# Performance work log

Hardware: AMD Instinct MI355X
Metric: run time of the kernel (lower is better)

## Reference

```python
import jax, jax.numpy as jnp
import numpy as np

N_NODES = 50000
N_EDGES = 800000
IN_CH = 128
HIDDEN = 32
HEADS = 4
OUT_CH = 128


def _lin_params(key, fan_in, fan_out):
    kw, kb = jax.random.split(key)
    scale = 1.0 / np.sqrt(fan_in)
    W = jax.random.uniform(kw, (fan_in, fan_out), minval=-scale, maxval=scale, dtype=jnp.float32)
    b = jax.random.uniform(kb, (fan_out,), minval=-scale, maxval=scale, dtype=jnp.float32)
    return W, b


def setup_inputs() -> dict:
    key = jax.random.key(0)
    ks = jax.random.split(key, 10)
    x = jax.random.normal(ks[0], (N_NODES, IN_CH), dtype=jnp.float32)
    edge_index = jax.random.randint(ks[1], (2, N_EDGES), 0, N_NODES, dtype=jnp.int64)
    d1 = HIDDEN * HEADS  # 128
    Wq1, bq1 = _lin_params(ks[2], IN_CH, d1)
    Wk1, bk1 = _lin_params(ks[3], IN_CH, d1)
    Wv1, bv1 = _lin_params(ks[4], IN_CH, d1)
    Ws1, bs1 = _lin_params(ks[5], IN_CH, d1)
    Wq2, bq2 = _lin_params(ks[6], d1, OUT_CH)
    Wk2, bk2 = _lin_params(ks[7], d1, OUT_CH)
    Wv2, bv2 = _lin_params(ks[8], d1, OUT_CH)
    Ws2, bs2 = _lin_params(ks[9], d1, OUT_CH)
    return dict(x=x, edge_index=edge_index,
                Wq1=Wq1, bq1=bq1, Wk1=Wk1, bk1=bk1, Wv1=Wv1, bv1=bv1, Ws1=Ws1, bs1=bs1,
                Wq2=Wq2, bq2=bq2, Wk2=Wk2, bk2=bk2, Wv2=Wv2, bv2=bv2, Ws2=Ws2, bs2=bs2)


def transformer_conv(x, src, dst, Wq, bq, Wk, bk, Wv, bv, Ws, bs, heads, n_nodes):
    """PyG TransformerConv (concat=True, beta=False, root_weight=True, dropout=0)."""
    H = heads
    d = Wq.shape[1] // H
    q = (x @ Wq + bq).reshape(n_nodes, H, d)  # [N,H,d]
    k = (x @ Wk + bk).reshape(n_nodes, H, d)
    v = (x @ Wv + bv).reshape(n_nodes, H, d)
    q_e = q[dst]          # [E,H,d] gather by destination (x_i)
    k_e = k[src]          # [E,H,d] gather by source (x_j)
    alpha = jnp.einsum('ehd,ehd->eh', q_e, k_e) / jnp.sqrt(jnp.float32(d))  # [E,H]
    # segment softmax over incoming edges of each destination node
    m = jax.ops.segment_max(alpha, dst, num_segments=n_nodes)  # [N,H]
    m = jnp.where(jnp.isfinite(m), m, 0.0)
    e = jnp.exp(alpha - m[dst])
    denom = jax.ops.segment_sum(e, dst, num_segments=n_nodes)  # [N,H]
    attn = e / (denom[dst] + 1e-16)                            # [E,H]
    msg = v[src] * attn[:, :, None]                            # [E,H,d]
    out = jax.ops.segment_sum(msg, dst, num_segments=n_nodes)  # [N,H,d]
    out = out.reshape(n_nodes, H * d)
    return out + (x @ Ws + bs)  # root/skip connection


def reference(x, edge_index, Wq1, bq1, Wk1, bk1, Wv1, bv1, Ws1, bs1,
              Wq2, bq2, Wk2, bk2, Wv2, bv2, Ws2, bs2):
    src = edge_index[0]
    dst = edge_index[1]
    n = x.shape[0]
    h = transformer_conv(x, src, dst, Wq1, bq1, Wk1, bk1, Wv1, bv1, Ws1, bs1, HEADS, n)
    h = jax.nn.relu(h)
    out = transformer_conv(h, src, dst, Wq2, bq2, Wk2, bk2, Wv2, bv2, Ws2, bs2, 1, n)
    return out
```

## Files before the change

kernel.cpp:

```cpp
#include <hip/hip_runtime.h>

#define N_NODES 50000
#define N_EDGES 800000

typedef __attribute__((ext_vector_type(8))) short bf16x8;
typedef __attribute__((ext_vector_type(4))) float f32x4;

__device__ inline unsigned short f2bf(float f) {
  unsigned int u = __float_as_uint(f);
  unsigned int r = u + 0x7FFFu + ((u >> 16) & 1u);
  return (unsigned short)(r >> 16);
}
__device__ inline float bf_lo(unsigned int u) { return __uint_as_float(u << 16); }
__device__ inline float bf_hi(unsigned int u) { return __uint_as_float(u & 0xffff0000u); }

__global__ void edges_prep(const int* __restrict__ ei,
                           int* __restrict__ src, int* __restrict__ dst,
                           int* __restrict__ cnt) {
  int e = blockIdx.x * 256 + threadIdx.x;
  int hi = ei[2 * e + 1];
  unsigned long long b = __ballot(hi == 0);
  bool is64 = (b == 0xFFFFFFFFFFFFFFFFull);
  int s, d;
  if (is64) { s = ei[2 * e]; d = ei[2 * (N_EDGES + e)]; }
  else      { s = ei[e];     d = ei[N_EDGES + e]; }
  src[e] = s; dst[e] = d;
  atomicAdd(&cnt[d], 1);
}

__device__ inline int block_excl_scan_256(int v, int& total) {
  __shared__ int lds[8];
  int lane = threadIdx.x & 63, wid = threadIdx.x >> 6;
  int orig = v;
#pragma unroll
  for (int off = 1; off < 64; off <<= 1) {
    int t = __shfl_up(v, off);
    if (lane >= off) v += t;
  }
  if (lane == 63) lds[wid] = v;
  __syncthreads();
  if (threadIdx.x == 0) {
    int s = 0;
    for (int w = 0; w < 4; ++w) { int t = lds[w]; lds[w] = s; s += t; }
    lds[4] = s;
  }
  __syncthreads();
  total = lds[4];
  return v + lds[wid] - orig;
}

__global__ __launch_bounds__(256) void scan1(const int* __restrict__ cnt,
                                             int* __restrict__ excl,
                                             int* __restrict__ partials) {
  int i = blockIdx.x * 256 + threadIdx.x;
  int v = (i < N_NODES) ? cnt[i] : 0;
  int total;
  int e = block_excl_scan_256(v, total);
  if (i < N_NODES) excl[i] = e;
  if (threadIdx.x == 0) partials[blockIdx.x] = total;
}

__global__ __launch_bounds__(256) void scan2(int* __restrict__ partials, int nb) {
  int i = threadIdx.x;
  int v = (i < nb) ? partials[i] : 0;
  int total;
  int e = block_excl_scan_256(v, total);
  if (i < nb) partials[i] = e;
}

__global__ __launch_bounds__(256) void scan3(int* __restrict__ row_ptr,
                                             const int* __restrict__ partials,
                                             int* __restrict__ cursor) {
  int i = blockIdx.x * 256 + threadIdx.x;
  if (i < N_NODES) {
    int v = row_ptr[i] + partials[blockIdx.x];
    row_ptr[i] = v;
    cursor[i] = v;
  }
  if (i == 0) row_ptr[N_NODES] = N_EDGES;
}

__global__ void scatter_k(const int* __restrict__ src, const int* __restrict__ dst,
                          int* __restrict__ cursor, int* __restrict__ ssrc) {
  int e = blockIdx.x * 256 + threadIdx.x;
  if (e < N_EDGES) {
    int p = atomicAdd(&cursor[dst[e]], 1);
    ssrc[p] = src[e];
  }
}

__global__ void prep_w(const float* __restrict__ Wq, const float* __restrict__ bq,
                       const float* __restrict__ Wk, const float* __restrict__ bk,
                       const float* __restrict__ Wv, const float* __restrict__ bv,
                       const float* __restrict__ Ws, const float* __restrict__ bs,
                       unsigned short* __restrict__ bt, float* __restrict__ bcat) {
  int t = blockIdx.x * 256 + threadIdx.x;
  int col = t >> 7, kk = t & 127;
  int sel = col >> 7, c = col & 127;
  const float* W = (sel == 0) ? Wq : (sel == 1) ? Wk : (sel == 2) ? Wv : Ws;
  bt[col * 128 + kk] = f2bf(W[kk * 128 + c]);
  if (kk == 0) {
    const float* B = (sel == 0) ? bq : (sel == 1) ? bk : (sel == 2) ? bv : bs;
    bcat[col] = B[c];
  }
}

template <bool AF32>
__global__ __launch_bounds__(256) void gemm_qkvs(const void* __restrict__ xa,
                                                 const unsigned short* __restrict__ bt,
                                                 const float* __restrict__ bias,
                                                 unsigned short* __restrict__ Oqs,
                                                 unsigned short* __restrict__ Okv) {
  const int wid = threadIdx.x >> 6;
  const int lane = threadIdx.x & 63;
  const int gw = blockIdx.x * 4 + wid;
  const int colGroup = gw & 7;
  const int rowGroup = gw >> 3;
  const int col0 = colGroup * 64;
  const int r = lane & 15;
  const int half = lane >> 4;

  bf16x8 bfrag[4][4];
#pragma unroll
  for (int ct = 0; ct < 4; ++ct) {
    int col = col0 + ct * 16 + r;
    const unsigned short* bp = bt + col * 128 + half * 8;
#pragma unroll
    for (int kc = 0; kc < 4; ++kc)
      bfrag[ct][kc] = *(const bf16x8*)(bp + kc * 32);
  }

#pragma unroll 1
  for (int rt = 0; rt < 5; ++rt) {
    int m0 = (rowGroup * 5 + rt) * 16;
    bf16x8 afrag[4];
    if constexpr (AF32) {
      const float* ap = (const float*)xa + (size_t)(m0 + r) * 128 + half * 8;
#pragma unroll
      for (int kc = 0; kc < 4; ++kc) {
        float4 f0 = *(const float4*)(ap + kc * 32);
        float4 f1 = *(const float4*)(ap + kc * 32 + 4);
        bf16x8 fr;
        fr[0] = (short)f2bf(f0.x); fr[1] = (short)f2bf(f0.y);
        fr[2] = (short)f2bf(f0.z); fr[3] = (short)f2bf(f0.w);
        fr[4] = (short)f2bf(f1.x); fr[5] = (short)f2bf(f1.y);
        fr[6] = (short)f2bf(f1.z); fr[7] = (short)f2bf(f1.w);
        afrag[kc] = fr;
      }
    } else {
      const unsigned short* ap = (const unsigned short*)xa + (size_t)(m0 + r) * 128 + half * 8;
#pragma unroll
      for (int kc = 0; kc < 4; ++kc) afrag[kc] = *(const bf16x8*)(ap + kc * 32);
    }

    f32x4 acc[4] = {{0.f,0.f,0.f,0.f},{0.f,0.f,0.f,0.f},{0.f,0.f,0.f,0.f},{0.f,0.f,0.f,0.f}};
#pragma unroll
    for (int ct = 0; ct < 4; ++ct)
#pragma unroll
      for (int kc = 0; kc < 4; ++kc)
        acc[ct] = __builtin_amdgcn_mfma_f32_16x16x32_bf16(afrag[kc], bfrag[ct][kc], acc[ct], 0, 0, 0);

    int orow = m0 + half * 4;
    if (colGroup < 2) {
#pragma unroll
      for (int ct = 0; ct < 4; ++ct) {
        int col = col0 + ct * 16 + r;
        float bv = bias[col];
#pragma unroll
        for (int j = 0; j < 4; ++j)
          Oqs[(size_t)(orow + j) * 256 + col] = f2bf(acc[ct][j] + bv);
      }
    } else if (colGroup >= 6) {
#pragma unroll
      for (int ct = 0; ct < 4; ++ct) {
        int col = col0 + ct * 16 + r;
        float bv = bias[col];
        int c = col - 384;
#pragma unroll
        for (int j = 0; j < 4; ++j)
          Oqs[(size_t)(orow + j) * 256 + 128 + c] = f2bf(acc[ct][j] + bv);
      }
    } else {
      const int voff  = (colGroup >= 4) ? 2 : 0;
      const int cbase = (colGroup >= 4) ? 256 : 128;
#pragma unroll
      for (int ct = 0; ct < 4; ++ct) {
        int col = col0 + ct * 16 + r;
        float bv = bias[col];
        int c = col - cbase;
        int pos = ((c >> 1) << 2) + voff + (c & 1);
#pragma unroll
        for (int j = 0; j < 4; ++j)
          Okv[(size_t)(orow + j) * 256 + pos] = f2bf(acc[ct][j] + bv);
      }
    }
  }
}

template <int H, bool OUTBF>
__global__ __launch_bounds__(256) void edge_attn(const unsigned short* __restrict__ Oqs,
                                                 const unsigned short* __restrict__ Okv,
                                                 const int* __restrict__ row_ptr,
                                                 const int* __restrict__ ssrc,
                                                 void* __restrict__ outp,
                                                 float scale) {
  int wid = threadIdx.x >> 6, lane = threadIdx.x & 63;
  int n = blockIdx.x * 4 + wid;
  if (n >= N_NODES) return;
  const unsigned int* qsw = (const unsigned int*)Oqs;
  unsigned int qw = qsw[(size_t)n * 128 + lane];
  float qx = bf_lo(qw) * scale, qy = bf_hi(qw) * scale;
  int start = row_ptr[n], end = row_ptr[n + 1];
  int len = end - start;
  const int* sp = ssrc + start;
  const uint2* kvb = (const uint2*)Okv;
  float acc0 = 0.f, acc1 = 0.f, den = 0.f;

  auto proc = [&](uint2 kv) {
    float p = qx * bf_lo(kv.x) + qy * bf_hi(kv.x);
#pragma unroll
    for (int off = 1; off < 64 / H; off <<= 1) p += __shfl_xor(p, off);
    float e = __expf(p);
    den += e; acc0 += e * bf_lo(kv.y); acc1 += e * bf_hi(kv.y);
  };

  int i = 0;
  if (len >= 4) {
    uint2 a = kvb[(size_t)sp[0] * 64 + lane];
    uint2 b = kvb[(size_t)sp[1] * 64 + lane];
    uint2 c = kvb[(size_t)sp[2] * 64 + lane];
    uint2 d = kvb[(size_t)sp[3] * 64 + lane];
    for (i = 4; i + 3 < len; i += 4) {
      uint2 na = kvb[(size_t)sp[i]     * 64 + lane];
      uint2 nb = kvb[(size_t)sp[i + 1] * 64 + lane];
      uint2 nc = kvb[(size_t)sp[i + 2] * 64 + lane];
      uint2 nd = kvb[(size_t)sp[i + 3] * 64 + lane];
      proc(a); proc(b); proc(c); proc(d);
      a = na; b = nb; c = nc; d = nd;
    }
    proc(a); proc(b); proc(c); proc(d);
  }
  for (; i < len; ++i) proc(kvb[(size_t)sp[i] * 64 + lane]);

  float inv = 1.0f / (den + 1e-16f);
  unsigned int sw = qsw[(size_t)n * 128 + 64 + lane];
  float r0 = acc0 * inv + bf_lo(sw);
  float r1 = acc1 * inv + bf_hi(sw);
  if (OUTBF) {
    r0 = fmaxf(r0, 0.f); r1 = fmaxf(r1, 0.f);
    unsigned int pk = (unsigned int)f2bf(r0) | ((unsigned int)f2bf(r1) << 16);
    ((unsigned int*)outp)[(size_t)n * 64 + lane] = pk;
  } else {
    ((float2*)outp)[(size_t)n * 64 + lane] = make_float2(r0, r1);
  }
}

extern "C" void kernel_launch(void* const* d_in, const int* in_sizes, int n_in,
                              void* d_out, int out_size, void* d_ws, size_t ws_size,
                              hipStream_t stream) {
  (void)in_sizes; (void)n_in; (void)out_size; (void)ws_size;
  const float* x  = (const float*)d_in[0];
  const int*   ei = (const int*)d_in[1];
  const float *Wq1 = (const float*)d_in[2],  *bq1 = (const float*)d_in[3];
  const float *Wk1 = (const float*)d_in[4],  *bk1 = (const float*)d_in[5];
  const float *Wv1 = (const float*)d_in[6],  *bv1 = (const float*)d_in[7];
  const float *Ws1 = (const float*)d_in[8],  *bs1 = (const float*)d_in[9];
  const float *Wq2 = (const float*)d_in[10], *bq2 = (const float*)d_in[11];
  const float *Wk2 = (const float*)d_in[12], *bk2 = (const float*)d_in[13];
  const float *Wv2 = (const float*)d_in[14], *bv2 = (const float*)d_in[15];
  const float *Ws2 = (const float*)d_in[16], *bs2 = (const float*)d_in[17];
  float* out = (float*)d_out;

  char* w = (char*)d_ws;
  size_t off = 0;
  auto alloc = [&](size_t b) { void* p = w + off; off += (b + 255) & ~(size_t)255; return p; };
  int* src    = (int*)alloc((size_t)N_EDGES * 4);
  int* dstA   = (int*)alloc((size_t)N_EDGES * 4);
  int* ssrc   = (int*)alloc((size_t)N_EDGES * 4);
  int* rowp   = (int*)alloc((size_t)(N_NODES + 1) * 4);
  int* cursor = (int*)alloc((size_t)N_NODES * 4);
  int* cnt    = (int*)alloc((size_t)N_NODES * 4);
  int* part   = (int*)alloc(256 * 4);
  unsigned short* xb  = (unsigned short*)alloc((size_t)N_NODES * 128 * 2);
  unsigned short* bt  = (unsigned short*)alloc((size_t)512 * 128 * 2);
  float* bcat = (float*)alloc(512 * 4);
  unsigned short* Oqs = (unsigned short*)alloc((size_t)N_NODES * 256 * 2);
  unsigned short* Okv = (unsigned short*)alloc((size_t)N_NODES * 256 * 2);

  hipMemsetAsync(cnt, 0, (size_t)N_NODES * 4, stream);
  edges_prep<<<3125, 256, 0, stream>>>(ei, src, dstA, cnt);
  scan1<<<196, 256, 0, stream>>>(cnt, rowp, part);
  scan2<<<1, 256, 0, stream>>>(part, 196);
  scan3<<<196, 256, 0, stream>>>(rowp, part, cursor);
  scatter_k<<<3125, 256, 0, stream>>>(src, dstA, cursor, ssrc);

  prep_w<<<256, 256, 0, stream>>>(Wq1, bq1, Wk1, bk1, Wv1, bv1, Ws1, bs1, bt, bcat);
  gemm_qkvs<true><<<1250, 256, 0, stream>>>(x, bt, bcat, Oqs, Okv);
  edge_attn<4, true><<<12500, 256, 0, stream>>>(Oqs, Okv, rowp, ssrc, xb, 0.17677669529663689f);

  prep_w<<<256, 256, 0, stream>>>(Wq2, bq2, Wk2, bk2, Wv2, bv2, Ws2, bs2, bt, bcat);
  gemm_qkvs<false><<<1250, 256, 0, stream>>>(xb, bt, bcat, Oqs, Okv);
  edge_attn<1, false><<<12500, 256, 0, stream>>>(Oqs, Okv, rowp, ssrc, out, 0.08838834764831845f);
}
```

Measured before the change: 407.3 us.

## Read edge_index directly in scatter, merge weight prep, use bf16 dot2 and deeper prefetch

Drops the intermediate src/dst arrays: the histogram and scatter kernels now read edge_index directly, so one write-then-reread pass goes away. Both layers' weight preparation is merged into one launch, removing a kernel. The edge attention kernel computes the q·k dot product with the bf16 fdot2 instruction when it is available, applies the scale after the shuffle reduction, raises the gather prefetch depth from 4 to 8 edges, and adds an occupancy hint to launch_bounds. The deeper prefetch and the occupancy hint both compete for registers, and nodes with fewer than 8 edges now fall through to the slower scalar tail loop.

```diff
diff --git a/kernel.cpp b/kernel.cpp
--- a/kernel.cpp
+++ b/kernel.cpp
@@ -5,6 +5,13 @@
 
 typedef __attribute__((ext_vector_type(8))) short bf16x8;
 typedef __attribute__((ext_vector_type(4))) float f32x4;
+
+#if __has_builtin(__builtin_amdgcn_fdot2_f32_bf16)
+#define HAVE_FDOT2 1
+typedef __attribute__((ext_vector_type(2))) __bf16 bf16v2;
+#else
+#define HAVE_FDOT2 0
+#endif
 
 __device__ inline unsigned short f2bf(float f) {
   unsigned int u = __float_as_uint(f);
@@ -14,18 +21,24 @@
 __device__ inline float bf_lo(unsigned int u) { return __uint_as_float(u << 16); }
 __device__ inline float bf_hi(unsigned int u) { return __uint_as_float(u & 0xffff0000u); }
 
-__global__ void edges_prep(const int* __restrict__ ei,
-                           int* __restrict__ src, int* __restrict__ dst,
-                           int* __restrict__ cnt) {
+__global__ void hist_direct(const int* __restrict__ ei, int* __restrict__ cnt) {
   int e = blockIdx.x * 256 + threadIdx.x;
   int hi = ei[2 * e + 1];
-  unsigned long long b = __ballot(hi == 0);
-  bool is64 = (b == 0xFFFFFFFFFFFFFFFFull);
+  bool is64 = (__ballot(hi == 0) == 0xFFFFFFFFFFFFFFFFull);
+  int d = is64 ? ei[2 * (N_EDGES + e)] : ei[N_EDGES + e];
+  atomicAdd(&cnt[d], 1);
+}
+
+__global__ void scatter_direct(const int* __restrict__ ei, int* __restrict__ cursor,
+                               int* __restrict__ ssrc) {
+  int e = blockIdx.x * 256 + threadIdx.x;
+  int hi = ei[2 * e + 1];
+  bool is64 = (__ballot(hi == 0) == 0xFFFFFFFFFFFFFFFFull);
   int s, d;
   if (is64) { s = ei[2 * e]; d = ei[2 * (N_EDGES + e)]; }
   else      { s = ei[e];     d = ei[N_EDGES + e]; }
-  src[e] = s; dst[e] = d;
-  atomicAdd(&cnt[d], 1);
+  int p = atomicAdd(&cursor[d], 1);
+  ssrc[p] = s;
 }
 
 __device__ inline int block_excl_scan_256(int v, int& total) {
@@ -80,29 +93,19 @@
   if (i == 0) row_ptr[N_NODES] = N_EDGES;
 }
 
-__global__ void scatter_k(const int* __restrict__ src, const int* __restrict__ dst,
-                          int* __restrict__ cursor, int* __restrict__ ssrc) {
-  int e = blockIdx.x * 256 + threadIdx.x;
-  if (e < N_EDGES) {
-    int p = atomicAdd(&cursor[dst[e]], 1);
-    ssrc[p] = src[e];
-  }
-}
-
-__global__ void prep_w(const float* __restrict__ Wq, const float* __restrict__ bq,
-                       const float* __restrict__ Wk, const float* __restrict__ bk,
-                       const float* __restrict__ Wv, const float* __restrict__ bv,
-                       const float* __restrict__ Ws, const float* __restrict__ bs,
-                       unsigned short* __restrict__ bt, float* __restrict__ bcat) {
+struct WPack { const float* W[8]; const float* B[8]; };
+
+__global__ void prep_w_both(WPack pk, unsigned short* __restrict__ bt_all,
+                            float* __restrict__ bcat_all) {
   int t = blockIdx.x * 256 + threadIdx.x;
-  int col = t >> 7, kk = t & 127;
+  int lay = t >> 16;
+  int r = t & 65535;
+  int col = r >> 7, kk = r & 127;
   int sel = col >> 7, c = col & 127;
-  const float* W = (sel == 0) ? Wq : (sel == 1) ? Wk : (sel == 2) ? Wv : Ws;
-  bt[col * 128 + kk] = f2bf(W[kk * 128 + c]);
-  if (kk == 0) {
-    const float* B = (sel == 0) ? bq : (sel == 1) ? bk : (sel == 2) ? bv : bs;
-    bcat[col] = B[c];
-  }
+  int idx = lay * 4 + sel;
+  const float* W = pk.W[idx];
+  bt_all[(size_t)lay * 65536 + col * 128 + kk] = f2bf(W[kk * 128 + c]);
+  if (kk == 0) bcat_all[lay * 512 + col] = pk.B[idx][c];
 }
 
 template <bool AF32>
@@ -198,18 +201,23 @@
 }
 
 template <int H, bool OUTBF>
-__global__ __launch_bounds__(256) void edge_attn(const unsigned short* __restrict__ Oqs,
-                                                 const unsigned short* __restrict__ Okv,
-                                                 const int* __restrict__ row_ptr,
-                                                 const int* __restrict__ ssrc,
-                                                 void* __restrict__ outp,
-                                                 float scale) {
+__global__ __launch_bounds__(256, 8) void edge_attn(const unsigned short* __restrict__ Oqs,
+                                                    const unsigned short* __restrict__ Okv,
+                                                    const int* __restrict__ row_ptr,
+                                                    const int* __restrict__ ssrc,
+                                                    void* __restrict__ outp,
+                                                    float scale) {
   int wid = threadIdx.x >> 6, lane = threadIdx.x & 63;
   int n = blockIdx.x * 4 + wid;
   if (n >= N_NODES) return;
   const unsigned int* qsw = (const unsigned int*)Oqs;
   unsigned int qw = qsw[(size_t)n * 128 + lane];
+#if HAVE_FDOT2
+  const float esc = scale;
+  bf16v2 qv = __builtin_bit_cast(bf16v2, qw);
+#else
   float qx = bf_lo(qw) * scale, qy = bf_hi(qw) * scale;
+#endif
   int start = row_ptr[n], end = row_ptr[n + 1];
   int len = end - start;
   const int* sp = ssrc + start;
@@ -217,28 +225,44 @@
   float acc0 = 0.f, acc1 = 0.f, den = 0.f;
 
   auto proc = [&](uint2 kv) {
+#if HAVE_FDOT2
+    float p = __builtin_amdgcn_fdot2_f32_bf16(__builtin_bit_cast(bf16v2, kv.x), qv, 0.f, false);
+#else
     float p = qx * bf_lo(kv.x) + qy * bf_hi(kv.x);
+#endif
 #pragma unroll
     for (int off = 1; off < 64 / H; off <<= 1) p += __shfl_xor(p, off);
+#if HAVE_FDOT2
+    float e = __expf(p * esc);
+#else
     float e = __expf(p);
+#endif
     den += e; acc0 += e * bf_lo(kv.y); acc1 += e * bf_hi(kv.y);
   };
 
   int i = 0;
-  if (len >= 4) {
+  if (len >= 8) {
     uint2 a = kvb[(size_t)sp[0] * 64 + lane];
     uint2 b = kvb[(size_t)sp[1] * 64 + lane];
     uint2 c = kvb[(size_t)sp[2] * 64 + lane];
     uint2 d = kvb[(size_t)sp[3] * 64 + lane];
-    for (i = 4; i + 3 < len; i += 4) {
+    uint2 e4 = kvb[(size_t)sp[4] * 64 + lane];
+    uint2 f = kvb[(size_t)sp[5] * 64 + lane];
+    uint2 g = kvb[(size_t)sp[6] * 64 + lane];
+    uint2 h = kvb[(size_t)sp[7] * 64 + lane];
+    for (i = 8; i + 7 < len; i += 8) {
       uint2 na = kvb[(size_t)sp[i]     * 64 + lane];
       uint2 nb = kvb[(size_t)sp[i + 1] * 64 + lane];
       uint2 nc = kvb[(size_t)sp[i + 2] * 64 + lane];
       uint2 nd = kvb[(size_t)sp[i + 3] * 64 + lane];
-      proc(a); proc(b); proc(c); proc(d);
-      a = na; b = nb; c = nc; d = nd;
+      uint2 ne = kvb[(size_t)sp[i + 4] * 64 + lane];
+      uint2 nf = kvb[(size_t)sp[i + 5] * 64 + lane];
+      uint2 ng = kvb[(size_t)sp[i + 6] * 64 + lane];
+      uint2 nh = kvb[(size_t)sp[i + 7] * 64 + lane];
+      proc(a); proc(b); proc(c); proc(d); proc(e4); proc(f); proc(g); proc(h);
+      a = na; b = nb; c = nc; d = nd; e4 = ne; f = nf; g = ng; h = nh;
     }
-    proc(a); proc(b); proc(c); proc(d);
+    proc(a); proc(b); proc(c); proc(d); proc(e4); proc(f); proc(g); proc(h);
   }
   for (; i < len; ++i) proc(kvb[(size_t)sp[i] * 64 + lane]);
 
@@ -261,44 +285,36 @@
   (void)in_sizes; (void)n_in; (void)out_size; (void)ws_size;
   const float* x  = (const float*)d_in[0];
   const int*   ei = (const int*)d_in[1];
-  const float *Wq1 = (const float*)d_in[2],  *bq1 = (const float*)d_in[3];
-  const float *Wk1 = (const float*)d_in[4],  *bk1 = (const float*)d_in[5];
-  const float *Wv1 = (const float*)d_in[6],  *bv1 = (const float*)d_in[7];
-  const float *Ws1 = (const float*)d_in[8],  *bs1 = (const float*)d_in[9];
-  const float *Wq2 = (const float*)d_in[10], *bq2 = (const float*)d_in[11];
-  const float *Wk2 = (const float*)d_in[12], *bk2 = (const float*)d_in[13];
-  const float *Wv2 = (const float*)d_in[14], *bv2 = (const float*)d_in[15];
-  const float *Ws2 = (const float*)d_in[16], *bs2 = (const float*)d_in[17];
   float* out = (float*)d_out;
 
   char* w = (char*)d_ws;
   size_t off = 0;
   auto alloc = [&](size_t b) { void* p = w + off; off += (b + 255) & ~(size_t)255; return p; };
-  int* src    = (int*)alloc((size_t)N_EDGES * 4);
-  int* dstA   = (int*)alloc((size_t)N_EDGES * 4);
   int* ssrc   = (int*)alloc((size_t)N_EDGES * 4);
   int* rowp   = (int*)alloc((size_t)(N_NODES + 1) * 4);
   int* cursor = (int*)alloc((size_t)N_NODES * 4);
   int* cnt    = (int*)alloc((size_t)N_NODES * 4);
   int* part   = (int*)alloc(256 * 4);
   unsigned short* xb  = (unsigned short*)alloc((size_t)N_NODES * 128 * 2);
-  unsigned short* bt  = (unsigned short*)alloc((size_t)512 * 128 * 2);
-  float* bcat = (float*)alloc(512 * 4);
+  unsigned short* bt  = (unsigned short*)alloc((size_t)2 * 512 * 128 * 2);
+  float* bcat = (float*)alloc(2 * 512 * 4);
   unsigned short* Oqs = (unsigned short*)alloc((size_t)N_NODES * 256 * 2);
   unsigned short* Okv = (unsigned short*)alloc((size_t)N_NODES * 256 * 2);
 
+  WPack pk;
+  for (int i = 0; i < 8; ++i) { pk.W[i] = (const float*)d_in[2 + 2 * i]; pk.B[i] = (const float*)d_in[3 + 2 * i]; }
+
   hipMemsetAsync(cnt, 0, (size_t)N_NODES * 4, stream);
-  edges_prep<<<3125, 256, 0, stream>>>(ei, src, dstA, cnt);
+  hist_direct<<<3125, 256, 0, stream>>>(ei, cnt);
   scan1<<<196, 256, 0, stream>>>(cnt, rowp, part);
   scan2<<<1, 256, 0, stream>>>(part, 196);
   scan3<<<196, 256, 0, stream>>>(rowp, part, cursor);
-  scatter_k<<<3125, 256, 0, stream>>>(src, dstA, cursor, ssrc);
-
-  prep_w<<<256, 256, 0, stream>>>(Wq1, bq1, Wk1, bk1, Wv1, bv1, Ws1, bs1, bt, bcat);
+  scatter_direct<<<3125, 256, 0, stream>>>(ei, cursor, ssrc);
+  prep_w_both<<<512, 256, 0, stream>>>(pk, bt, bcat);
+
   gemm_qkvs<true><<<1250, 256, 0, stream>>>(x, bt, bcat, Oqs, Okv);
   edge_attn<4, true><<<12500, 256, 0, stream>>>(Oqs, Okv, rowp, ssrc, xb, 0.17677669529663689f);
 
-  prep_w<<<256, 256, 0, stream>>>(Wq2, bq2, Wk2, bk2, Wv2, bv2, Ws2, bs2, bt, bcat);
-  gemm_qkvs<false><<<1250, 256, 0, stream>>>(xb, bt, bcat, Oqs, Okv);
+  gemm_qkvs<false><<<1250, 256, 0, stream>>>(xb, bt + 65536, bcat + 512, Oqs, Okv);
   edge_attn<1, false><<<12500, 256, 0, stream>>>(Oqs, Okv, rowp, ssrc, out, 0.08838834764831845f);
 }
```

Measured after the change: 404.1 us. Within noise of the previous version (-0.8%).
